# Optimization experiments

Hardware: AMD Instinct MI355X
Metric: run time of the kernel (lower is better)

The kernel has to match this reference:

```python
import jax, jax.numpy as jnp
import numpy as np

N_USER = 50000
N_ITEM = 50000
E = 500000
D = 256
H = 8
DK = D // H
EPS = 1e-5
SQRT_DK = float(np.sqrt(DK))


def _layernorm(x, g, b):
    m = jnp.mean(x, axis=-1, keepdims=True)
    v = jnp.var(x, axis=-1, keepdims=True)
    return (x - m) * jax.lax.rsqrt(v + EPS) * g + b


def _etype_aggregate(h_src, h_dst, src, dst, n_dst, Wk, bk, Wq, bq, Wv, bv, pri, att, msg):
    # per-ntype K/Q/V projections, then per-relation head-wise transforms
    k = (h_src @ Wk + bk).reshape(-1, H, DK)
    v = (h_src @ Wv + bv).reshape(-1, H, DK)
    q = (h_dst @ Wq + bq).reshape(-1, H, DK)
    k = jnp.einsum('nhi,hij->nhj', k, att)
    v = jnp.einsum('nhi,hij->nhj', v, msg)
    # v_dot_u score per edge per head: [E, H]
    score = jnp.einsum('ehd,ehd->eh', q[dst], k[src]) * pri / SQRT_DK
    # edge_softmax normalized per destination node (per head)
    smax = jax.ops.segment_max(score, dst, num_segments=n_dst)
    ex = jnp.exp(score - smax[dst])
    ssum = jax.ops.segment_sum(ex, dst, num_segments=n_dst)
    a = ex / ssum[dst]
    # u_mul_e + sum reduce (zero-in-degree dst nodes get zeros, like DGL sum)
    t = jax.ops.segment_sum(v[src] * a[:, :, None], dst, num_segments=n_dst)
    return t.reshape(n_dst, D)


def _dst_update(t, h, Wa, ba, skip, g, b):
    alpha = jax.nn.sigmoid(skip)
    out = (t @ Wa + ba) * alpha + h * (1.0 - alpha)
    return _layernorm(out, g, b)


def _forward(h_user, h_item, src_ui, dst_ui, src_iu, dst_iu, Wk_user, bk_user, Wq_user, bq_user, Wv_user, bv_user, Wa_user, ba_user, ln_g_user, ln_b_user, skip_user, Wk_item, bk_item, Wq_item, bq_item, Wv_item, bv_item, Wa_item, ba_item, ln_g_item, ln_b_item, skip_item, pri_ui, att_ui, msg_ui, pri_iu, att_iu, msg_iu):
    # (user, click, item): k/v from src ntype 'user', q from dst ntype 'item'
    t_item = _etype_aggregate(h_user, h_item, src_ui, dst_ui, N_ITEM, Wk_user, bk_user, Wq_item, bq_item, Wv_user, bv_user, pri_ui, att_ui, msg_ui)
    # (item, rev_click, user)
    t_user = _etype_aggregate(h_item, h_user, src_iu, dst_iu, N_USER, Wk_item, bk_item, Wq_user, bq_user, Wv_item, bv_item, pri_iu, att_iu, msg_iu)
    # each ntype is dst of exactly one etype -> cross_reducer 'mean' is identity
    new_user = _dst_update(t_user, h_user, Wa_user, ba_user, skip_user, ln_g_user, ln_b_user)
    new_item = _dst_update(t_item, h_item, Wa_item, ba_item, skip_item, ln_g_item, ln_b_item)
    return jnp.stack([new_user, new_item])  # [2, N, D]


def setup_inputs() -> dict:
    key = jax.random.key(0)
    ks = jax.random.split(key, 16)

    def xavier(k, shape):
        s = np.sqrt(2.0 / (shape[-2] + shape[-1]))
        return (jax.random.normal(k, shape, dtype=jnp.float32) * s).astype(jnp.float32)

    inp = {}
    inp['h_user'] = jax.random.normal(ks[0], (N_USER, D), dtype=jnp.float32)
    inp['h_item'] = jax.random.normal(ks[1], (N_ITEM, D), dtype=jnp.float32)
    inp['src_ui'] = jax.random.randint(ks[2], (E,), 0, N_USER, dtype=jnp.int32)
    inp['dst_ui'] = jax.random.randint(ks[3], (E,), 0, N_ITEM, dtype=jnp.int32)
    inp['src_iu'] = jax.random.randint(ks[4], (E,), 0, N_ITEM, dtype=jnp.int32)
    inp['dst_iu'] = jax.random.randint(ks[5], (E,), 0, N_USER, dtype=jnp.int32)
    i = 6
    for nt in ['user', 'item']:
        for nm in ['k', 'q', 'v', 'a']:
            inp[f'W{nm}_{nt}'] = xavier(jax.random.fold_in(ks[i], hash(nm) % 1000), (D, D))
            inp[f'b{nm}_{nt}'] = jnp.zeros((D,), jnp.float32)
        i += 1
        inp[f'ln_g_{nt}'] = jnp.ones((D,), jnp.float32)
        inp[f'ln_b_{nt}'] = jnp.zeros((D,), jnp.float32)
        inp[f'skip_{nt}'] = jnp.ones((1,), jnp.float32)
    for et in ['ui', 'iu']:
        inp[f'pri_{et}'] = jnp.ones((H,), jnp.float32)
        inp[f'att_{et}'] = xavier(ks[i], (H, DK, DK)); i += 1
        inp[f'msg_{et}'] = xavier(ks[i], (H, DK, DK)); i += 1
    return inp


def reference(h_user, h_item, src_ui, dst_ui, src_iu, dst_iu, Wk_user, bk_user, Wq_user, bq_user, Wv_user, bv_user, Wa_user, ba_user, ln_g_user, ln_b_user, skip_user, Wk_item, bk_item, Wq_item, bq_item, Wv_item, bv_item, Wa_item, ba_item, ln_g_item, ln_b_item, skip_item, pri_ui, att_ui, msg_ui, pri_iu, att_iu, msg_iu):
    return _forward(h_user, h_item, src_ui, dst_ui, src_iu, dst_iu, Wk_user, bk_user, Wq_user, bq_user, Wv_user, bv_user, Wa_user, ba_user, ln_g_user, ln_b_user, skip_user, Wk_item, bk_item, Wq_item, bq_item, Wv_item, bv_item, Wa_item, ba_item, ln_g_item, ln_b_item, skip_item, pri_ui, att_ui, msg_ui, pri_iu, att_iu, msg_iu)
```

## Files before the change

kernel.cpp:

```cpp
#include <hip/hip_runtime.h>

#define NN 50000
#define DD 256
#define HH 8
#define EE 500000
#define INV_SQRT_DK 0.17677669529663687f

typedef __attribute__((ext_vector_type(8))) short bf16x8;
typedef __attribute__((ext_vector_type(4))) float f32x4;

__device__ __forceinline__ unsigned short f2bf(float f) {
    unsigned int u = __float_as_uint(f);
    u = (u + 0x7FFFu + ((u >> 16) & 1u)) >> 16;
    return (unsigned short)u;
}
__device__ __forceinline__ float bf2f(unsigned short u) {
    return __uint_as_float(((unsigned int)u) << 16);
}
__device__ __forceinline__ float bflo(unsigned int u) {
    return __uint_as_float(u << 16);
}
__device__ __forceinline__ float bfhi(unsigned int u) {
    return __uint_as_float(u & 0xFFFF0000u);
}

__global__ __launch_bounds__(256) void conv_bf16(const float* __restrict__ Xu,
                                                 const float* __restrict__ Xi,
                                                 unsigned short* __restrict__ Yu,
                                                 unsigned short* __restrict__ Yi) {
    const size_t ND = (size_t)NN * DD;
    size_t i = ((size_t)blockIdx.x * 256 + threadIdx.x) * 4;
    const float* X = Xu; unsigned short* Y = Yu;
    if (i >= ND) { X = Xi; Y = Yi; i -= ND; }
    float4 v = *(const float4*)&X[i];
    ushort4 o;
    o.x = f2bf(v.x); o.y = f2bf(v.y); o.z = f2bf(v.z); o.w = f2bf(v.w);
    *(ushort4*)&Y[i] = o;
}

__global__ __launch_bounds__(256) void fuse_kernel(const float* __restrict__ Wk_u, const float* __restrict__ bk_u,
                                                   const float* __restrict__ att_ui_,
                                                   const float* __restrict__ Wv_u, const float* __restrict__ bv_u,
                                                   const float* __restrict__ msg_ui_,
                                                   const float* __restrict__ Wk_i, const float* __restrict__ bk_i,
                                                   const float* __restrict__ att_iu_,
                                                   const float* __restrict__ Wv_i, const float* __restrict__ bv_i,
                                                   const float* __restrict__ msg_iu_,
                                                   unsigned short* __restrict__ BTu, float* __restrict__ beffU,
                                                   unsigned short* __restrict__ BTi, float* __restrict__ beffI) {
    int y = blockIdx.y;
    const float* W = (y == 0) ? Wk_u : (y == 1) ? Wv_u : (y == 2) ? Wk_i : Wv_i;
    const float* b = (y == 0) ? bk_u : (y == 1) ? bv_u : (y == 2) ? bk_i : bv_i;
    const float* T = (y == 0) ? att_ui_ : (y == 1) ? msg_ui_ : (y == 2) ? att_iu_ : msg_iu_;
    unsigned short* WT = (y < 2) ? BTu : BTi;
    float* be = (y < 2) ? beffU : beffI;
    int j = threadIdx.x;
    int h = j >> 5, jj = j & 31;
    int pj = ((j >> 2) << 3) + (j & 3) + ((y & 1) ? 4 : 0);
    const float* Th = T + h * 1024;
    if (blockIdx.x < 256) {
        int c = blockIdx.x;
        float acc = 0.f;
        #pragma unroll 8
        for (int i = 0; i < 32; ++i) acc += W[c * 256 + h * 32 + i] * Th[i * 32 + jj];
        WT[pj * 256 + c] = f2bf(acc);
    } else {
        float acc = 0.f;
        #pragma unroll 8
        for (int i = 0; i < 32; ++i) acc += b[h * 32 + i] * Th[i * 32 + jj];
        be[pj] = acc;
    }
}

__global__ __launch_bounds__(256) void convT_kernel(const float* __restrict__ Wq_u, const float* __restrict__ bq_u,
                                                    const float* __restrict__ Wq_i, const float* __restrict__ bq_i,
                                                    const float* __restrict__ Wa_u, const float* __restrict__ Wa_i,
                                                    unsigned short* __restrict__ BTu, float* __restrict__ beffU,
                                                    unsigned short* __restrict__ BTi, float* __restrict__ beffI,
                                                    unsigned short* __restrict__ WaTu, unsigned short* __restrict__ WaTi) {
    int y = blockIdx.y;
    const float* W = (y == 0) ? Wq_u : (y == 1) ? Wq_i : (y == 2) ? Wa_u : Wa_i;
    unsigned short* WT = (y == 0) ? BTu + 512 * 256 : (y == 1) ? BTi + 512 * 256 : (y == 2) ? WaTu : WaTi;
    int k = blockIdx.x, n = threadIdx.x;
    WT[n * 256 + k] = f2bf(W[k * 256 + n]);
    if (k == 0 && y < 2) {
        float* be = (y == 0) ? beffU : beffI;
        const float* bq = (y == 0) ? bq_u : bq_i;
        be[512 + n] = bq[n];
    }
}

__global__ void hist_kernel(const int* __restrict__ dst_ui, const int* __restrict__ dst_iu,
                            int* __restrict__ cnt) {
    int e = blockIdx.x * blockDim.x + threadIdx.x;
    if (e < EE) atomicAdd(&cnt[dst_ui[e]], 1);
    else if (e < 2 * EE) atomicAdd(&cnt[NN + dst_iu[e - EE]], 1);
}

__global__ __launch_bounds__(256) void alloc_kernel(const int* __restrict__ cnt,
                                                    int* __restrict__ start,
                                                    int* __restrict__ ctr) {
    int y = blockIdx.y;
    int i = blockIdx.x * 256 + threadIdx.x;
    int idx = y * NN + i;
    int v = (i < NN) ? cnt[idx] : 0;
    int lane = threadIdx.x & 63;
    int pre = v;
    #pragma unroll
    for (int o = 1; o < 64; o <<= 1) {
        int u = __shfl_up(pre, o, 64);
        if (lane >= o) pre += u;
    }
    int wsum = __shfl(pre, 63, 64);
    int base = 0;
    if (lane == 63) base = atomicAdd(&ctr[y], wsum);
    base = __shfl(base, 63, 64);
    if (i < NN) start[idx] = y * EE + base + pre - v;
}

__global__ void scatter_kernel(const int* __restrict__ dst_ui, const int* __restrict__ src_ui,
                               const int* __restrict__ dst_iu, const int* __restrict__ src_iu,
                               const int* __restrict__ start, int* __restrict__ cur,
                               int* __restrict__ srcid) {
    int e = blockIdx.x * blockDim.x + threadIdx.x;
    int d, s;
    if (e < EE) { d = dst_ui[e]; s = src_ui[e]; }
    else if (e < 2 * EE) { d = NN + dst_iu[e - EE]; s = src_iu[e - EE]; }
    else return;
    int pos = start[d] + atomicAdd(&cur[d], 1);
    srcid[pos] = s;
}

__global__ __launch_bounds__(256) void gemm_kvq(const unsigned short* __restrict__ Au,
                                                const unsigned short* __restrict__ Ai,
                                                const unsigned short* __restrict__ BTu,
                                                const unsigned short* __restrict__ BTi,
                                                const float* __restrict__ beffU,
                                                const float* __restrict__ beffI,
                                                unsigned short* __restrict__ KVu,
                                                unsigned short* __restrict__ KVi,
                                                unsigned short* __restrict__ Qu,
                                                unsigned short* __restrict__ Qi) {
    __shared__ __align__(16) char smem[20480];
    bf16x8* As = (bf16x8*)smem;
    bf16x8* Bs = (bf16x8*)(smem + 10240);
    int z = blockIdx.z;
    const unsigned short* A = z ? Ai : Au;
    const unsigned short* BT = z ? BTi : BTu;
    const float* beff = z ? beffI : beffU;
    unsigned short* KV = z ? KVi : KVu;
    unsigned short* Qb = z ? Qi : Qu;
    int bm = blockIdx.x * 128, bn = blockIdx.y * 128;
    int tid = threadIdx.x;
    int lane = tid & 63, w = tid >> 6;
    int wm = (w & 1) * 64, wn = (w >> 1) * 64;
    int m16 = lane & 15, q = lane >> 4;
    f32x4 acc[4][4] = {};
    for (int k0 = 0; k0 < 256; k0 += 32) {
        #pragma unroll
        for (int cc = 0; cc < 2; ++cc) {
            int c = tid + cc * 256;
            int row = c >> 2, off8 = c & 3;
            int gr = bm + row;
            bf16x8 va = {};
            if (gr < NN) va = *(const bf16x8*)&A[(size_t)gr * 256 + k0 + off8 * 8];
            As[row * 5 + off8] = va;
            Bs[row * 5 + off8] = *(const bf16x8*)&BT[(size_t)(bn + row) * 256 + k0 + off8 * 8];
        }
        __syncthreads();
        bf16x8 af[4], bfr[4];
        #pragma unroll
        for (int i = 0; i < 4; ++i) af[i] = As[(wm + 16 * i + m16) * 5 + q];
        #pragma unroll
        for (int j = 0; j < 4; ++j) bfr[j] = Bs[(wn + 16 * j + m16) * 5 + q];
        #pragma unroll
        for (int i = 0; i < 4; ++i)
            #pragma unroll
            for (int j = 0; j < 4; ++j)
                acc[i][j] = __builtin_amdgcn_mfma_f32_16x16x32_bf16(af[i], bfr[j], acc[i][j], 0, 0, 0);
        __syncthreads();
    }
    const bool isKV = (bn < 512);
    unsigned short* dstb = isKV ? KV : Qb;
    const int rowlen = isKV ? 512 : 256;
    const int coloff = isKV ? bn : (bn - 512);
    unsigned short* Cs = (unsigned short*)smem;
    #pragma unroll
    for (int half = 0; half < 2; ++half) {
        if ((w & 1) == half) {
            #pragma unroll
            for (int i = 0; i < 4; ++i) {
                int rloc = 16 * i + q * 4;
                #pragma unroll
                for (int j = 0; j < 4; ++j) {
                    int cl = wn + 16 * j + m16;
                    float bv = beff[bn + cl];
                    #pragma unroll
                    for (int r = 0; r < 4; ++r)
                        Cs[(rloc + r) * 136 + cl] = f2bf(acc[i][j][r] + bv);
                }
            }
        }
        __syncthreads();
        #pragma unroll
        for (int it = 0; it < 4; ++it) {
            int idx = it * 256 + tid;
            int row = idx >> 4, seg = idx & 15;
            int gr = bm + half * 64 + row;
            if (gr < NN) {
                bf16x8 v = *(const bf16x8*)&Cs[row * 136 + seg * 8];
                *(bf16x8*)&dstb[(size_t)gr * rowlen + coloff + seg * 8] = v;
            }
        }
        __syncthreads();
    }
}

__global__ __launch_bounds__(512) void gemm_ln(const unsigned short* __restrict__ A0,
                                               const unsigned short* __restrict__ A1,
                                               const unsigned short* __restrict__ BT0,
                                               const unsigned short* __restrict__ BT1,
                                               const float* __restrict__ ba0,
                                               const float* __restrict__ ba1,
                                               const float* __restrict__ h0,
                                               const float* __restrict__ h1,
                                               const float* __restrict__ skp0,
                                               const float* __restrict__ skp1,
                                               const float* __restrict__ g0, const float* __restrict__ be0,
                                               const float* __restrict__ g1, const float* __restrict__ be1,
                                               float* __restrict__ out) {
    __shared__ __align__(16) char smem[33280];
    bf16x8* As = (bf16x8*)smem;
    bf16x8* Bs = (bf16x8*)(smem + 10240);
    float* Es = (float*)smem;
    int z = blockIdx.y;
    const unsigned short* A = z ? A1 : A0;
    const unsigned short* BT = z ? BT1 : BT0;
    const float* ba = z ? ba1 : ba0;
    const float* hb = z ? h1 : h0;
    const float* skp = z ? skp1 : skp0;
    const float* g = z ? g1 : g0;
    const float* bb = z ? be1 : be0;
    float* o = out + (z ? (size_t)NN * DD : 0);

    int bm = blockIdx.x * 128;
    int tid = threadIdx.x;
    int lane = tid & 63, w = tid >> 6;
    int m16 = lane & 15, q = lane >> 4;
    f32x4 acc[16] = {};
    for (int k0 = 0; k0 < 256; k0 += 32) {
        {
            int row = tid >> 2, ch = tid & 3;
            int gr = bm + row;
            bf16x8 va = {};
            if (gr < NN) va = *(const bf16x8*)&A[(size_t)gr * 256 + k0 + ch * 8];
            As[row * 5 + ch] = va;
        }
        #pragma unroll
        for (int cc = 0; cc < 2; ++cc) {
            int idx = tid + cc * 512;
            int n = idx >> 2, ch = idx & 3;
            Bs[n * 5 + ch] = *(const bf16x8*)&BT[(size_t)n * 256 + k0 + ch * 8];
        }
        __syncthreads();
        bf16x8 af = As[(w * 16 + m16) * 5 + q];
        #pragma unroll
        for (int jh = 0; jh < 2; ++jh) {
            bf16x8 bfr[8];
            #pragma unroll
            for (int jj = 0; jj < 8; ++jj) bfr[jj] = Bs[((jh * 8 + jj) * 16 + m16) * 5 + q];
            #pragma unroll
            for (int jj = 0; jj < 8; ++jj)
                acc[jh * 8 + jj] = __builtin_amdgcn_mfma_f32_16x16x32_bf16(af, bfr[jj], acc[jh * 8 + jj], 0, 0, 0);
        }
        __syncthreads();
    }
    float alpha = 1.f / (1.f + __expf(-skp[0]));
    float am1 = 1.f - alpha;
    float4 ba4 = *(const float4*)&ba[lane * 4];
    float4 g4 = *(const float4*)&g[lane * 4];
    float4 b4 = *(const float4*)&bb[lane * 4];
    #pragma unroll
    for (int p = 0; p < 4; ++p) {
        if ((w >> 1) == p) {
            int rbase = (w & 1) * 16 + 4 * q;
            #pragma unroll
            for (int j = 0; j < 16; ++j)
                #pragma unroll
                for (int rr = 0; rr < 4; ++rr)
                    Es[(rbase + rr) * 260 + 16 * j + m16] = acc[j][rr];
        }
        __syncthreads();
        #pragma unroll
        for (int rrr = 0; rrr < 4; ++rrr) {
            int lrow = w * 4 + rrr;
            int gr = bm + 32 * p + lrow;
            if (gr < NN) {
                float4 tm = *(const float4*)&Es[lrow * 260 + lane * 4];
                float4 hh = *(const float4*)&hb[(size_t)gr * 256 + lane * 4];
                float x0 = (tm.x + ba4.x) * alpha + hh.x * am1;
                float x1 = (tm.y + ba4.y) * alpha + hh.y * am1;
                float x2 = (tm.z + ba4.z) * alpha + hh.z * am1;
                float x3 = (tm.w + ba4.w) * alpha + hh.w * am1;
                float s = x0 + x1 + x2 + x3;
                #pragma unroll
                for (int off = 32; off > 0; off >>= 1) s += __shfl_xor(s, off, 64);
                float mean = s * (1.f / 256.f);
                float d0 = x0 - mean, d1 = x1 - mean, d2 = x2 - mean, d3 = x3 - mean;
                float s2 = d0 * d0 + d1 * d1 + d2 * d2 + d3 * d3;
                #pragma unroll
                for (int off = 32; off > 0; off >>= 1) s2 += __shfl_xor(s2, off, 64);
                float rstd = rsqrtf(s2 * (1.f / 256.f) + 1e-5f);
                float4 r;
                r.x = d0 * rstd * g4.x + b4.x;
                r.y = d1 * rstd * g4.y + b4.y;
                r.z = d2 * rstd * g4.z + b4.z;
                r.w = d3 * rstd * g4.w + b4.w;
                *(float4*)&o[(size_t)gr * 256 + lane * 4] = r;
            }
        }
        __syncthreads();
    }
}

__global__ __launch_bounds__(256) void fused_agg(const int* __restrict__ start,
                                                 const int* __restrict__ cnt,
                                                 const int* __restrict__ srcid,
                                                 const unsigned short* __restrict__ Qi,
                                                 const unsigned short* __restrict__ Qu,
                                                 const unsigned short* __restrict__ KVu,
                                                 const unsigned short* __restrict__ KVi,
                                                 const float* __restrict__ pri_ui,
                                                 const float* __restrict__ pri_iu,
                                                 unsigned short* __restrict__ tI16,
                                                 unsigned short* __restrict__ tU16) {
    int w = threadIdx.x >> 6;
    int lane = threadIdx.x & 63;
    int b = blockIdx.x * 4 + w;
    bool second = (b >= NN);
    int d = second ? b - NN : b;
    const unsigned short* Q = second ? Qu : Qi;
    const unsigned short* KV = second ? KVi : KVu;
    const float* pri = second ? pri_iu : pri_ui;
    unsigned short* T = second ? tU16 : tI16;

    int h = lane >> 3;
    float sscale = pri[h] * INV_SQRT_DK;
    ushort4 q4 = *(const ushort4*)&Q[(size_t)d * 256 + lane * 4];
    float qx = bf2f(q4.x), qy = bf2f(q4.y), qz = bf2f(q4.z), qw = bf2f(q4.w);

    int p0 = start[b], n = cnt[b];
    float a0 = 0.f, a1 = 0.f, a2 = 0.f, a3 = 0.f, l = 0.f;

#define LDKV(idx) (*(const uint4*)&KV[(size_t)__shfl(myS, (idx), 64) * 512 + lane * 8])
#define PROC(kv) { \
        float sc = qx * bflo(kv.x) + qy * bfhi(kv.x) + qz * bflo(kv.y) + qw * bfhi(kv.y); \
        sc += __shfl_xor(sc, 1, 8); \
        sc += __shfl_xor(sc, 2, 8); \
        sc += __shfl_xor(sc, 4, 8); \
        float wgt = __expf(sc * sscale); \
        a0 += wgt * bflo(kv.z); \
        a1 += wgt * bfhi(kv.z); \
        a2 += wgt * bflo(kv.w); \
        a3 += wgt * bfhi(kv.w); \
        l += wgt; }

    for (int base = 0; base < n; base += 64) {
        int rem = n - base; if (rem > 64) rem = 64;
        int myS = (lane < rem) ? srcid[p0 + base + lane] : 0;
        uint4 k0 = {}, k1 = {}, k2 = {}, k3 = {};
        if (0 < rem) k0 = LDKV(0);
        if (1 < rem) k1 = LDKV(1);
        if (2 < rem) k2 = LDKV(2);
        if (3 < rem) k3 = LDKV(3);
        int t = 0;
        for (; t + 4 <= rem; t += 4) {
            PROC(k0); if (t + 4 < rem) k0 = LDKV(t + 4);
            PROC(k1); if (t + 5 < rem) k1 = LDKV(t + 5);
            PROC(k2); if (t + 6 < rem) k2 = LDKV(t + 6);
            PROC(k3); if (t + 7 < rem) k3 = LDKV(t + 7);
        }
        if (t < rem)     PROC(k0);
        if (t + 1 < rem) PROC(k1);
        if (t + 2 < rem) PROC(k2);
    }
#undef LDKV
#undef PROC

    float inv = (l > 0.f) ? 1.f / l : 0.f;
    ushort4 o;
    o.x = f2bf(a0 * inv); o.y = f2bf(a1 * inv);
    o.z = f2bf(a2 * inv); o.w = f2bf(a3 * inv);
    *(ushort4*)&T[(size_t)d * 256 + lane * 4] = o;
}

extern "C" void kernel_launch(void* const* d_in, const int* in_sizes, int n_in,
                              void* d_out, int out_size, void* d_ws, size_t ws_size,
                              hipStream_t stream) {
    const float* h_user  = (const float*)d_in[0];
    const float* h_item  = (const float*)d_in[1];
    const int*   src_ui  = (const int*)d_in[2];
    const int*   dst_ui  = (const int*)d_in[3];
    const int*   src_iu  = (const int*)d_in[4];
    const int*   dst_iu  = (const int*)d_in[5];
    const float* Wk_user = (const float*)d_in[6];
    const float* bk_user = (const float*)d_in[7];
    const float* Wq_user = (const float*)d_in[8];
    const float* bq_user = (const float*)d_in[9];
    const float* Wv_user = (const float*)d_in[10];
    const float* bv_user = (const float*)d_in[11];
    const float* Wa_user = (const float*)d_in[12];
    const float* ba_user = (const float*)d_in[13];
    const float* ln_g_user = (const float*)d_in[14];
    const float* ln_b_user = (const float*)d_in[15];
    const float* skip_user = (const float*)d_in[16];
    const float* Wk_item = (const float*)d_in[17];
    const float* bk_item = (const float*)d_in[18];
    const float* Wq_item = (const float*)d_in[19];
    const float* bq_item = (const float*)d_in[20];
    const float* Wv_item = (const float*)d_in[21];
    const float* bv_item = (const float*)d_in[22];
    const float* Wa_item = (const float*)d_in[23];
    const float* ba_item = (const float*)d_in[24];
    const float* ln_g_item = (const float*)d_in[25];
    const float* ln_b_item = (const float*)d_in[26];
    const float* skip_item = (const float*)d_in[27];
    const float* pri_ui = (const float*)d_in[28];
    const float* att_ui = (const float*)d_in[29];
    const float* msg_ui = (const float*)d_in[30];
    const float* pri_iu = (const float*)d_in[31];
    const float* att_iu = (const float*)d_in[32];
    const float* msg_iu = (const float*)d_in[33];
    float* out = (float*)d_out;

    const size_t ND = (size_t)NN * DD;

    unsigned short* up = (unsigned short*)d_ws;
    unsigned short* KVu = up;  up += (size_t)NN * 512;
    unsigned short* KVi = up;  up += (size_t)NN * 512;
    unsigned short* Qu  = up;  up += ND;
    unsigned short* Qi  = up;  up += ND;
    unsigned short* hU16 = up; up += ND;
    unsigned short* hI16 = up; up += ND;
    unsigned short* BTu = up;  up += 768 * 256;
    unsigned short* BTi = up;  up += 768 * 256;
    unsigned short* WaTu = up; up += 65536;
    unsigned short* WaTi = up; up += 65536;
    float* fp = (float*)up;
    float* beffU = fp; fp += 768;
    float* beffI = fp; fp += 768;
    int* ip = (int*)fp;
    int* cnt   = ip; ip += 2 * NN;
    int* cur   = ip; ip += 2 * NN;
    int* ctr   = ip; ip += 2;
    int* start = ip; ip += 2 * NN;
    int* srcid = ip; ip += 2 * EE;
    unsigned short* tU16 = hU16;
    unsigned short* tI16 = hI16;

    const int eb = (EE + 255) / 256;

    conv_bf16<<<2 * 12500, 256, 0, stream>>>(h_user, h_item, hU16, hI16);
    fuse_kernel<<<dim3(257, 4), 256, 0, stream>>>(Wk_user, bk_user, att_ui, Wv_user, bv_user, msg_ui,
                                                  Wk_item, bk_item, att_iu, Wv_item, bv_item, msg_iu,
                                                  BTu, beffU, BTi, beffI);
    convT_kernel<<<dim3(256, 4), 256, 0, stream>>>(Wq_user, bq_user, Wq_item, bq_item, Wa_user, Wa_item,
                                                   BTu, beffU, BTi, beffI, WaTu, WaTi);
    hipMemsetAsync(cnt, 0, (4 * NN + 2) * sizeof(int), stream);
    hist_kernel<<<2 * eb, 256, 0, stream>>>(dst_ui, dst_iu, cnt);
    alloc_kernel<<<dim3(196, 2), 256, 0, stream>>>(cnt, start, ctr);
    scatter_kernel<<<2 * eb, 256, 0, stream>>>(dst_ui, src_ui, dst_iu, src_iu, start, cur, srcid);

    gemm_kvq<<<dim3(391, 6, 2), 256, 0, stream>>>(hU16, hI16, BTu, BTi, beffU, beffI,
                                                  KVu, KVi, Qu, Qi);

    fused_agg<<<25000, 256, 0, stream>>>(start, cnt, srcid, Qi, Qu, KVu, KVi,
                                         pri_ui, pri_iu, tI16, tU16);

    gemm_ln<<<dim3(391, 2), 512, 0, stream>>>(tU16, tI16, WaTu, WaTi, ba_user, ba_item,
                                              h_user, h_item, skip_user, skip_item,
                                              ln_g_user, ln_b_user, ln_g_item, ln_b_item, out);
}
```

Baseline: 693.9 us.

## Double-buffer LDS tiles with register prefetch in KVQ GEMM and swap grid order

The KVQ projection GEMM now keeps two LDS tile buffers and prefetches the next K-slice from global memory into registers while MFMA runs on the current slice, which cuts the synchronisation stalls between load and compute. The grid axes are also swapped so the six N-tiles of the same row block are launched next to each other, improving L2 reuse of the A rows. This doubles LDS use to 40 KB and adds register pressure, which may lower occupancy. The hunk shown no longer has the trailing __syncthreads of the old loop, so correctness depends on the unseen loop end.

```diff
diff --git a/kernel.cpp b/kernel.cpp
--- a/kernel.cpp
+++ b/kernel.cpp
@@ -141,38 +141,70 @@
                                                 unsigned short* __restrict__ KVi,
                                                 unsigned short* __restrict__ Qu,
                                                 unsigned short* __restrict__ Qi) {
-    __shared__ __align__(16) char smem[20480];
-    bf16x8* As = (bf16x8*)smem;
-    bf16x8* Bs = (bf16x8*)(smem + 10240);
+    __shared__ __align__(16) char smem[40960];
+    bf16x8* As0 = (bf16x8*)smem;
+    bf16x8* Bs0 = (bf16x8*)(smem + 10240);
+    bf16x8* As1 = (bf16x8*)(smem + 20480);
+    bf16x8* Bs1 = (bf16x8*)(smem + 30720);
     int z = blockIdx.z;
     const unsigned short* A = z ? Ai : Au;
     const unsigned short* BT = z ? BTi : BTu;
     const float* beff = z ? beffI : beffU;
     unsigned short* KV = z ? KVi : KVu;
     unsigned short* Qb = z ? Qi : Qu;
-    int bm = blockIdx.x * 128, bn = blockIdx.y * 128;
+    int bm = blockIdx.y * 128, bn = blockIdx.x * 128;
     int tid = threadIdx.x;
     int lane = tid & 63, w = tid >> 6;
     int wm = (w & 1) * 64, wn = (w >> 1) * 64;
     int m16 = lane & 15, q = lane >> 4;
+
+    int row0 = tid >> 2, off = tid & 3;
+    int row1 = row0 + 64;
+    int gr0 = bm + row0, gr1 = bm + row1;
+    const bool val0 = gr0 < NN, val1 = gr1 < NN;
+    const unsigned short* pA0 = &A[(size_t)gr0 * 256 + off * 8];
+    const unsigned short* pA1 = &A[(size_t)gr1 * 256 + off * 8];
+    const unsigned short* pB0 = &BT[(size_t)(bn + row0) * 256 + off * 8];
+    const unsigned short* pB1 = &BT[(size_t)(bn + row1) * 256 + off * 8];
+
     f32x4 acc[4][4] = {};
-    for (int k0 = 0; k0 < 256; k0 += 32) {
-        #pragma unroll
-        for (int cc = 0; cc < 2; ++cc) {
-            int c = tid + cc * 256;
-            int row = c >> 2, off8 = c & 3;
-            int gr = bm + row;
-            bf16x8 va = {};
-            if (gr < NN) va = *(const bf16x8*)&A[(size_t)gr * 256 + k0 + off8 * 8];
-            As[row * 5 + off8] = va;
-            Bs[row * 5 + off8] = *(const bf16x8*)&BT[(size_t)(bn + row) * 256 + k0 + off8 * 8];
-        }
-        __syncthreads();
+    const bf16x8 zz = {};
+    bf16x8 ra0 = zz, ra1 = zz, rb0, rb1;
+    if (val0) ra0 = *(const bf16x8*)pA0;
+    if (val1) ra1 = *(const bf16x8*)pA1;
+    rb0 = *(const bf16x8*)pB0;
+    rb1 = *(const bf16x8*)pB1;
+    As0[row0 * 5 + off] = ra0; As0[row1 * 5 + off] = ra1;
+    Bs0[row0 * 5 + off] = rb0; Bs0[row1 * 5 + off] = rb1;
+    ra0 = zz; ra1 = zz;
+    if (val0) ra0 = *(const bf16x8*)(pA0 + 32);
+    if (val1) ra1 = *(const bf16x8*)(pA1 + 32);
+    rb0 = *(const bf16x8*)(pB0 + 32);
+    rb1 = *(const bf16x8*)(pB1 + 32);
+    __syncthreads();
+    #pragma unroll
+    for (int ks = 0; ks < 8; ++ks) {
+        bf16x8* Ac = (ks & 1) ? As1 : As0;
+        bf16x8* Bc = (ks & 1) ? Bs1 : Bs0;
+        bf16x8* An = (ks & 1) ? As0 : As1;
+        bf16x8* Bn = (ks & 1) ? Bs0 : Bs1;
+        if (ks < 7) {
+            An[row0 * 5 + off] = ra0; An[row1 * 5 + off] = ra1;
+            Bn[row0 * 5 + off] = rb0; Bn[row1 * 5 + off] = rb1;
+        }
+        if (ks < 6) {
+            int k0 = (ks + 2) * 32;
+            ra0 = zz; ra1 = zz;
+            if (val0) ra0 = *(const bf16x8*)(pA0 + k0);
+            if (val1) ra1 = *(const bf16x8*)(pA1 + k0);
+            rb0 = *(const bf16x8*)(pB0 + k0);
+            rb1 = *(const bf16x8*)(pB1 + k0);
+        }
         bf16x8 af[4], bfr[4];
         #pragma unroll
-        for (int i = 0; i < 4; ++i) af[i] = As[(wm + 16 * i + m16) * 5 + q];
-        #pragma unroll
-        for (int j = 0; j < 4; ++j) bfr[j] = Bs[(wn + 16 * j + m16) * 5 + q];
+        for (int i = 0; i < 4; ++i) af[i] = Ac[(wm + 16 * i + m16) * 5 + q];
+        #pragma unroll
+        for (int j = 0; j < 4; ++j) bfr[j] = Bc[(wn + 16 * j + m16) * 5 + q];
         #pragma unroll
         for (int i = 0; i < 4; ++i)
             #pragma unroll
@@ -471,7 +503,7 @@
     alloc_kernel<<<dim3(196, 2), 256, 0, stream>>>(cnt, start, ctr);
     scatter_kernel<<<2 * eb, 256, 0, stream>>>(dst_ui, src_ui, dst_iu, src_iu, start, cur, srcid);
 
-    gemm_kvq<<<dim3(391, 6, 2), 256, 0, stream>>>(hU16, hI16, BTu, BTi, beffU, beffI,
+    gemm_kvq<<<dim3(6, 391, 2), 256, 0, stream>>>(hU16, hI16, BTu, BTi, beffU, beffI,
                                                   KVu, KVi, Qu, Qi);
 
     fused_agg<<<25000, 256, 0, stream>>>(start, cnt, srcid, Qi, Qu, KVu, KVi,
```

After: 672.6 us. 3.1% less time.
